# Performance work log

Measured on AMD Instinct MI355X. Metric: run time of the kernel, lower is better.

Reference implementation:

```python
import jax, jax.numpy as jnp
import numpy as np

BS, NV, D, DFF, E, H = 32, 512, 128, 512, 8, 8
EPS = 1e-5

def layernorm(x, g, b):
    m = x.mean(-1, keepdims=True)
    v = ((x - m) ** 2).mean(-1, keepdims=True)
    return (x - m) / jnp.sqrt(v + EPS) * g + b

def setup_inputs() -> dict:
    key = jax.random.key(0)
    ks = jax.random.split(key, 10)
    s = lambda k, shape: (jax.random.normal(k, shape, jnp.float32) * 0.02)
    return {
        "x": jax.random.normal(ks[0], (BS, NV, D), jnp.float32),
        "cls_emd": jax.random.normal(ks[1], (E, D), jnp.float32),
        "Wq": s(ks[2], (D, D)), "Wk": s(ks[3], (D, D)),
        "Wv": s(ks[4], (D, D)), "Wo": s(ks[5], (D, D)),
        "Wg": s(ks[6], (D, D)),
        "W1": s(ks[7], (E, DFF, 2 * D)), "b1": jnp.zeros((E, DFF), jnp.float32),
        "W2": s(ks[8], (E, D, DFF)), "b2": jnp.zeros((E, D), jnp.float32),
        "g1": jnp.ones((D,), jnp.float32), "be1": jnp.zeros((D,), jnp.float32),
        "g2": jnp.ones((D,), jnp.float32), "be2": jnp.zeros((D,), jnp.float32),
    }

def reference(x, cls_emd, Wq, Wk, Wv, Wo, Wg, W1, b1, W2, b2, g1, be1, g2, be2):
    bs, n, d = x.shape
    dh = d // H
    # --- full multi-head self-attention over the variate axis ---
    q = (x @ Wq).reshape(bs, n, H, dh)
    k = (x @ Wk).reshape(bs, n, H, dh)
    v = (x @ Wv).reshape(bs, n, H, dh)
    scores = jnp.einsum('bnhd,bmhd->bhnm', q, k) * (1.0 / np.sqrt(dh))
    attn = jax.nn.softmax(scores, axis=-1)            # [bs, H, n, n]
    new_x = jnp.einsum('bhnm,bmhd->bnhd', attn, v).reshape(bs, n, d) @ Wo
    # residual + norm1 (dropout = identity in eval)
    x = layernorm(x + new_x, g1, be1)
    # --- gating: per-variate scores over clusters [n_vars, n_clusters] ---
    gate_scores = jax.nn.softmax((x.mean(0) @ Wg) @ cls_emd.T, axis=-1)
    # --- MoE: expand tokens vs every cluster, concat, per-cluster expert MLP ---
    ncl = cls_emd.shape[0]
    y = jnp.broadcast_to(x[:, :, None, :], (bs, n, ncl, d))
    z = jnp.broadcast_to(cls_emd[None, None, :, :], (bs, n, ncl, d))
    yz_cat = jnp.concatenate([y, z], axis=-1)          # [bs, n, K, 2d]
    h = jax.nn.relu(jnp.einsum('bnkc,kfc->bnkf', yz_cat, W1) + b1)  # kernel_size=1 conv == matmul
    expert_out = jnp.einsum('bnkf,kdf->bnkd', h, W2) + b2           # [bs, n, K, d]
    y_r = jnp.einsum('nk,bnkd->bnd', gate_scores, expert_out)
    out = layernorm(x + y_r, g2, be2)
    return (out, attn, gate_scores)
```

## Files before the change

### kernel.cpp

```cpp
#include <hip/hip_runtime.h>
#include <hip/hip_bf16.h>
#include <math.h>

#define BS   32
#define NV   512
#define D    128
#define DFF  512
#define E    8
#define NH   8
#define DH   16
#define M_TOK (BS*NV)
#define EPS  1e-5f

typedef __hip_bfloat16 bf16;
typedef _Float16 f16;
using sh8   = __attribute__((ext_vector_type(8))) short;
using us4   = __attribute__((ext_vector_type(4))) unsigned short;
using h4    = __attribute__((ext_vector_type(4))) _Float16;
using h8    = __attribute__((ext_vector_type(8))) _Float16;
using f32x4 = __attribute__((ext_vector_type(4))) float;
using f32x16 = __attribute__((ext_vector_type(16))) float;

__device__ __forceinline__ float b2f(bf16 v){ return __bfloat162float(v); }
__device__ __forceinline__ bf16  f2b(float v){ return __float2bfloat16(v); }
__device__ __forceinline__ unsigned short f2bu(float v){
    bf16 b = __float2bfloat16(v);
    return __builtin_bit_cast(unsigned short, b);
}

__device__ __forceinline__ void gload_lds16(const void* g, void* l){
    __builtin_amdgcn_global_load_lds(
        (const __attribute__((address_space(1))) unsigned int*)g,
        (__attribute__((address_space(3))) unsigned int*)l, 16, 0, 0);
}

#define PR0 4096
#define PR1 (PR0 + 262144)
#define PR2 (PR1 + 131072)
#define PR3 (PR2 + 524288)
#define PR4 (PR3 + 49152)
#define PR5 (PR4 + 16384)
#define PREP_ITEMS PR5
__global__ __launch_bounds__(256) void k_prep(
    const float* __restrict__ W1, const float* __restrict__ W2,
    const float* __restrict__ x,  const float* __restrict__ Wq,
    const float* __restrict__ Wk, const float* __restrict__ Wv,
    const float* __restrict__ Wo, const float* __restrict__ b1,
    const float* __restrict__ cls,
    bf16* __restrict__ W1b, bf16* __restrict__ W2b, f16* __restrict__ xh,
    f16* __restrict__ WTq, f16* __restrict__ WoT, float* __restrict__ b1eff)
{
    int tid = blockIdx.x*256 + threadIdx.x;
    if (tid < PR0){
        int e = tid >> 9, f = tid & 511;
        float acc = b1[e*DFF + f];
        const float* wrow = W1 + ((size_t)e*DFF + f)*(2*D) + D;
        #pragma unroll 8
        for (int c=0;c<D;++c) acc += cls[e*D+c] * wrow[c];
        b1eff[tid] = acc;
    } else if (tid < PR1){
        int i = (tid - PR0)*4;
        float4 vv = *(const float4*)(W1 + i);
        us4 o; o[0]=f2bu(vv.x); o[1]=f2bu(vv.y); o[2]=f2bu(vv.z); o[3]=f2bu(vv.w);
        *(us4*)(W1b + i) = o;
    } else if (tid < PR2){
        int i = (tid - PR1)*4;
        float4 vv = *(const float4*)(W2 + i);
        us4 o; o[0]=f2bu(vv.x); o[1]=f2bu(vv.y); o[2]=f2bu(vv.z); o[3]=f2bu(vv.w);
        *(us4*)(W2b + i) = o;
    } else if (tid < PR3){
        int i = (tid - PR2)*4;
        float4 vv = *(const float4*)(x + i);
        h4 o; o[0]=(f16)vv.x; o[1]=(f16)vv.y; o[2]=(f16)vv.z; o[3]=(f16)vv.w;
        *(h4*)(xh + i) = o;
    } else if (tid < PR4){
        int idx = tid - PR3;
        int c = idx>>7, kk = idx&127;
        int which = c>>7, col = c&127;
        const float* W = which==0?Wq:(which==1?Wk:Wv);
        WTq[idx] = (f16)W[kk*D + col];
    } else if (tid < PR5){
        int idx = tid - PR4;
        int c = idx>>7, kk = idx&127;
        WoT[idx] = (f16)Wo[kk*D + c];
    }
}

__global__ __launch_bounds__(512) void k_qkv_mfma(
    const f16* __restrict__ xh, const f16* __restrict__ WT,
    f16* __restrict__ q, f16* __restrict__ k, f16* __restrict__ v)
{
    __shared__ __align__(16) char smem[65536];
    char* Xl = smem;
    char* Wl = smem + 16384;
    int t = threadIdx.x;
    int w = t>>6, lane = t&63;
    int bm = blockIdx.x, nh = blockIdx.y;

    const f16* xsrc = xh + (size_t)bm*64*D;
    #pragma unroll
    for (int i=0;i<2;++i){
        int ci = i*512 + t;
        int row = ci>>4, c16 = (ci&15)^(row&7);
        gload_lds16(xsrc + row*D + c16*8, Xl + (size_t)(i*512 + w*64)*16);
    }
    const f16* wsrc = WT + (size_t)nh*192*D;
    #pragma unroll
    for (int i=0;i<6;++i){
        int ci = i*512 + t;
        int row = ci>>4, c16 = (ci&15)^(row&7);
        gload_lds16(wsrc + row*D + c16*8, Wl + (size_t)(i*512 + w*64)*16);
    }
    __syncthreads();

    int rblk = w>>1, ch = w&1;
    int rl = lane&15, g = lane>>4;

    h8 afr[4];
    #pragma unroll
    for (int kk=0;kk<4;++kk){
        int row = rblk*16 + rl;
        int bo = (row<<8) + (kk<<6) + (g<<4); bo ^= (row&7)<<4;
        afr[kk] = *(const h8*)(Xl + bo);
    }
    f32x4 acc[6];
    #pragma unroll
    for (int nt=0;nt<6;++nt) acc[nt] = (f32x4){0.f,0.f,0.f,0.f};
    #pragma unroll
    for (int nt=0; nt<6; ++nt){
        #pragma unroll
        for (int kk=0;kk<4;++kk){
            int row = ch*96 + nt*16 + rl;
            int bo = (row<<8)+(kk<<6)+(g<<4); bo ^= (row&7)<<4;
            h8 bfr = *(const h8*)(Wl + bo);
            acc[nt] = __builtin_amdgcn_mfma_f32_16x16x32_f16(afr[kk], bfr, acc[nt],0,0,0);
        }
    }
    #pragma unroll
    for (int nt=0;nt<6;++nt){
        int cidx = nh*192 + ch*96 + nt*16 + rl;
        int which = cidx>>7, hh=(cidx>>4)&7, d = cidx&15;
        f16* dst = which==0?q:(which==1?k:v);
        #pragma unroll
        for (int j=0;j<4;++j){
            int m = bm*64 + rblk*16 + g*4 + j;
            int b = m>>9, n = m&511;
            dst[(((size_t)(b*NH+hh))*NV + n)*DH + d] = (f16)acc[nt][j];
        }
    }
}

#define KSTRIDE 24
#define VSTRIDE 520
#define PSTRIDE 68
__global__ __launch_bounds__(256) void k_attn2(
    const f16* __restrict__ q, const f16* __restrict__ kin, const f16* __restrict__ vin,
    float* __restrict__ attn_out, f16* __restrict__ ctx)
{
    __shared__ f16  Kl[512*KSTRIDE];
    __shared__ f16  VT[16*VSTRIDE];
    __shared__ f16  pbh[4][16*PSTRIDE];

    int bh = blockIdx.x;
    int t  = threadIdx.x;
    const f16* kb = kin + (size_t)bh*NV*DH;
    const f16* vb = vin + (size_t)bh*NV*DH;

    {
        int r0 = t*2;
        #pragma unroll
        for (int rr=0; rr<2; ++rr){
            const uint4* src = (const uint4*)(kb + (size_t)(r0+rr)*DH);
            *((uint4*)(Kl + (r0+rr)*KSTRIDE))     = src[0];
            *((uint4*)(Kl + (r0+rr)*KSTRIDE + 8)) = src[1];
        }
        const unsigned short* v0s = (const unsigned short*)(vb + (size_t)r0*DH);
        const unsigned short* v1s = v0s + DH;
        #pragma unroll
        for (int d=0; d<DH; ++d){
            unsigned u = (unsigned)v0s[d] | ((unsigned)v1s[d] << 16);
            *((unsigned*)(VT + d*VSTRIDE + r0)) = u;
        }
    }
    __syncthreads();

    int wave = t >> 6, lane = t & 63;
    int ql = lane & 15, g = lane >> 4;
    int q0 = blockIdx.y*64 + wave*16;

    h4 qf = *(const h4*)(q + ((size_t)bh*NV + q0 + ql)*DH + 4*g);
    #pragma unroll
    for (int i=0;i<4;++i) qf[i] = qf[i] * (_Float16)0.36067376f;

    f32x4 S[32];
    #pragma unroll
    for (int tt=0; tt<32; ++tt){
        h4 kf = *(const h4*)(Kl + (tt*16 + ql)*KSTRIDE + 4*g);
        S[tt] = __builtin_amdgcn_mfma_f32_16x16x16f16(kf, qf, (f32x4){0.f,0.f,0.f,0.f}, 0,0,0);
    }

    float sum = 0.f;
    #pragma unroll
    for (int tt=0; tt<32; ++tt)
        #pragma unroll
        for (int j=0;j<4;++j){
            float p = exp2f(S[tt][j]);
            S[tt][j] = p; sum += p;
        }
    sum += __shfl_xor(sum, 16);
    sum += __shfl_xor(sum, 32);
    float inv = 1.f/sum;
    #pragma unroll
    for (int tt=0; tt<32; ++tt)
        #pragma unroll
        for (int j=0;j<4;++j) S[tt][j] *= inv;

    f32x4 o0 = (f32x4){0.f,0.f,0.f,0.f}, o1 = (f32x4){0.f,0.f,0.f,0.f};
    f16* pw = pbh[wave];
    float* attnbase = attn_out + ((size_t)bh*NV + q0)*NV;
    int col16 = lane & 15, qg = lane >> 4;
    #pragma unroll
    for (int c=0; c<8; ++c){
        #pragma unroll
        for (int tt2=0; tt2<4; ++tt2){
            int tt = c*4 + tt2;
            h4 pf;
            pf[0]=(f16)S[tt][0]; pf[1]=(f16)S[tt][1];
            pf[2]=(f16)S[tt][2]; pf[3]=(f16)S[tt][3];
            h4 vf = *(const h4*)(VT + ql*VSTRIDE + tt*16 + 4*g);
            if (tt&1) o1 = __builtin_amdgcn_mfma_f32_16x16x16f16(vf, pf, o1, 0,0,0);
            else      o0 = __builtin_amdgcn_mfma_f32_16x16x16f16(vf, pf, o0, 0,0,0);
            *(h4*)(pw + ql*PSTRIDE + tt2*16 + 4*g) = pf;
        }
        asm volatile("" ::: "memory");
        #pragma unroll
        for (int rr=0; rr<4; ++rr){
            int qq = rr*4 + qg;
            h4 hv = *(const h4*)(pw + qq*PSTRIDE + col16*4);
            f32x4 vv;
            vv[0]=(float)hv[0]; vv[1]=(float)hv[1];
            vv[2]=(float)hv[2]; vv[3]=(float)hv[3];
            __builtin_nontemporal_store(vv, (f32x4*)(attnbase + (size_t)qq*NV + c*64 + col16*4));
        }
        asm volatile("" ::: "memory");
    }
    f32x4 o = o0 + o1;
    int b = bh >> 3, h = bh & 7;
    f16* cb = ctx + ((size_t)(b*NV) + q0 + ql)*D + h*DH + 4*g;
    h4 oc; oc[0]=(f16)o[0]; oc[1]=(f16)o[1]; oc[2]=(f16)o[2]; oc[3]=(f16)o[3];
    *(h4*)cb = oc;
}

__global__ __launch_bounds__(512) void k_woln_mfma(
    const f16* __restrict__ ctx, const f16* __restrict__ WoT,
    const float* __restrict__ x, const float* __restrict__ g1, const float* __restrict__ be1,
    bf16* __restrict__ x1b, float* __restrict__ yacc)
{
    __shared__ __align__(16) char smem[49152];
    __shared__ float lnred[2][64][2];
    char* Cl = smem;
    char* Wl = smem + 16384;
    int t = threadIdx.x;
    int w = t>>6, lane = t&63;
    int bm = blockIdx.x;

    const f16* csrc = ctx + (size_t)bm*64*D;
    #pragma unroll
    for (int i=0;i<2;++i){
        int ci = i*512 + t;
        int row = ci>>4, c16 = (ci&15)^(row&7);
        gload_lds16(csrc + row*D + c16*8, Cl + (size_t)(i*512 + w*64)*16);
    }
    #pragma unroll
    for (int i=0;i<4;++i){
        int ci = i*512 + t;
        int row = ci>>4, c16 = (ci&15)^(row&7);
        gload_lds16(WoT + row*D + c16*8, Wl + (size_t)(i*512 + w*64)*16);
    }
    __syncthreads();

    int rblk = w>>1, ch = w&1;
    int rl = lane&15, g = lane>>4;

    h8 afr[4];
    #pragma unroll
    for (int kk=0;kk<4;++kk){
        int row = rblk*16 + rl;
        int bo = (row<<8) + (kk<<6) + (g<<4); bo ^= (row&7)<<4;
        afr[kk] = *(const h8*)(Cl + bo);
    }
    f32x4 acc[4];
    #pragma unroll
    for (int nt=0;nt<4;++nt) acc[nt] = (f32x4){0.f,0.f,0.f,0.f};
    #pragma unroll
    for (int nt=0; nt<4; ++nt){
        #pragma unroll
        for (int kk=0;kk<4;++kk){
            int row = ch*64 + nt*16 + rl;
            int bo = (row<<8)+(kk<<6)+(g<<4); bo ^= (row&7)<<4;
            h8 bfr = *(const h8*)(Wl + bo);
            acc[nt] = __builtin_amdgcn_mfma_f32_16x16x32_f16(afr[kk], bfr, acc[nt],0,0,0);
        }
    }

    float rowv[4][4];
    #pragma unroll
    for (int j=0;j<4;++j){
        int m = bm*64 + rblk*16 + g*4 + j;
        #pragma unroll
        for (int dt=0;dt<4;++dt){
            int d = ch*64 + dt*16 + rl;
            rowv[j][dt] = acc[dt][j] + x[(size_t)m*D + d];
        }
    }
    #pragma unroll
    for (int j=0;j<4;++j){
        float s  = rowv[j][0]+rowv[j][1]+rowv[j][2]+rowv[j][3];
        float s2 = rowv[j][0]*rowv[j][0]+rowv[j][1]*rowv[j][1]
                 + rowv[j][2]*rowv[j][2]+rowv[j][3]*rowv[j][3];
        #pragma unroll
        for (int o=1;o<16;o<<=1){ s += __shfl_xor(s,o); s2 += __shfl_xor(s2,o); }
        if (rl==0){
            int row = rblk*16 + g*4 + j;
            lnred[ch][row][0] = s;
            lnred[ch][row][1] = s2;
        }
    }
    __syncthreads();
    #pragma unroll
    for (int j=0;j<4;++j){
        int row = rblk*16 + g*4 + j;
        float S  = lnred[0][row][0] + lnred[1][row][0];
        float S2 = lnred[0][row][1] + lnred[1][row][1];
        float mean = S*(1.f/D);
        float var  = S2*(1.f/D) - mean*mean;
        float rs = rsqrtf(var + EPS);
        int m = bm*64 + row;
        #pragma unroll
        for (int dt=0;dt<4;++dt){
            int d = ch*64 + dt*16 + rl;
            float o1 = (rowv[j][dt]-mean)*rs*g1[d] + be1[d];
            x1b[(size_t)m*D + d] = f2b(o1);
            yacc[(size_t)m*D + d] = o1;
        }
    }
}

__global__ __launch_bounds__(128) void k_gate(
    const float* __restrict__ yacc, const float* __restrict__ Wg, const float* __restrict__ cls,
    float* __restrict__ gate, float* __restrict__ gate_out)
{
    __shared__ float xm[D];
    __shared__ float tt[D];
    __shared__ float se[E];
    int n = blockIdx.x, t = threadIdx.x;
    float s = 0.f;
    #pragma unroll
    for (int b=0;b<BS;++b) s += yacc[((size_t)b*NV + n)*D + t];
    xm[t] = s * (1.f/BS);
    __syncthreads();
    float a = 0.f;
    for (int c=0;c<D;++c) a += xm[c] * Wg[c*D + t];
    tt[t] = a;
    __syncthreads();
    if (t < E){
        float acc=0.f;
        for (int c=0;c<D;++c) acc += tt[c] * cls[t*D + c];
        se[t]=acc;
    }
    __syncthreads();
    if (t==0){
        float mx=se[0];
        for(int e=1;e<E;++e) mx=fmaxf(mx,se[e]);
        float sm=0.f; float p[E];
        for(int e=0;e<E;++e){ p[e]=__expf(se[e]-mx); sm+=p[e]; }
        float inv=1.f/sm;
        for(int e=0;e<E;++e){
            gate[n*E+e]     = p[e]*inv;
            gate_out[n*E+e] = p[e]*inv;
        }
    }
}

__global__ __launch_bounds__(512) void k_moe_fused(
    const bf16* __restrict__ x1b, const bf16* __restrict__ W1b, const bf16* __restrict__ W2b,
    const float* __restrict__ b1eff, const float* __restrict__ b2,
    const float* __restrict__ gate, const float* __restrict__ yacc,
    const float* __restrict__ g2, const float* __restrict__ be2,
    float* __restrict__ out)
{
    __shared__ __align__(16) char smem[147456];
    char* Hl = smem + 131072;
    float (*lnred)[4][2] = (float (*)[4][2])Hl;

    int t = threadIdx.x;
    int w = t >> 6, lane = t & 63;
    int mb = w >> 2, nb = w & 3;
    int l31 = lane & 31, h = lane >> 5;
    int bm = blockIdx.x;

    sh8 afr[8];
    {
        const bf16* Ab = x1b + (size_t)(bm*64 + mb*32 + l31)*D;
        #pragma unroll
        for (int s=0;s<8;++s) afr[s] = *(const sh8*)(Ab + s*16 + h*8);
    }

    f32x16 oacc = {};
    f32x16 acc2e = {};

    auto STAGE = [&](int idx, int buf){
        int e = idx >> 2, fc = idx & 3;
        const bf16* w1src = W1b + ((size_t)e*DFF + fc*128)*(2*D);
        const bf16* w2src = W2b + (size_t)e*D*DFF + fc*128;
        char* Wa = smem + buf*65536;
        char* Wb = Wa + 32768;
        #pragma unroll
        for (int i=0;i<4;++i){
            int ci  = (i*8 + w)*64 + lane;
            int row = ci >> 4;
            int c16 = (ci & 15) ^ (row & 7);
            gload_lds16(w1src + (size_t)row*256 + c16*8, Wa + (size_t)(i*8+w)*1024);
            gload_lds16(w2src + (size_t)row*512 + c16*8, Wb + (size_t)(i*8+w)*1024);
        }
    };

    STAGE(0, 0);
    asm volatile("s_waitcnt vmcnt(0)" ::: "memory");
    __syncthreads();

    for (int idx=0; idx<32; ++idx){
        int buf = idx & 1;
        int e = idx >> 2, fc = idx & 3;
        char* Wa = smem + buf*65536;
        char* Wb = Wa + 32768;

        if (idx < 31) STAGE(idx+1, buf^1);

        f32x16 acc1 = {};
        {
            int row = nb*32 + l31;
            int rbase = (row<<8);
            int swz = (row&7)<<4;
            #pragma unroll
            for (int s=0;s<8;++s){
                int bo = (rbase + s*32 + h*16) ^ swz;
                sh8 bfr = *(const sh8*)(Wa + bo);
                acc1 = __builtin_amdgcn_mfma_f32_32x32x16_bf16(afr[s], bfr, acc1, 0,0,0);
            }
        }
        {
            float bia = b1eff[e*DFF + fc*128 + nb*32 + l31];
            #pragma unroll
            for (int r=0;r<16;++r){
                int rowm = mb*32 + (r&3) + 8*(r>>2) + 4*h;
                float v = acc1[r] + bia;
                v = v > 0.f ? v : 0.f;
                int bo = (rowm<<8) + ((nb*32 + l31)<<1);
                bo ^= (rowm&7)<<4;
                *(bf16*)(Hl + bo) = f2b(v);
            }
        }
        __syncthreads();

        {
            int rowh = mb*32 + l31;
            int hbase = (rowh<<8), hswz = (rowh&7)<<4;
            int roww = nb*32 + l31;
            int wbase = (roww<<8), wswz = (roww&7)<<4;
            #pragma unroll
            for (int s=0;s<8;++s){
                sh8 hfr = *(const sh8*)(Hl + ((hbase + s*32 + h*16) ^ hswz));
                sh8 wfr = *(const sh8*)(Wb + ((wbase + s*32 + h*16) ^ wswz));
                acc2e = __builtin_amdgcn_mfma_f32_32x32x16_bf16(hfr, wfr, acc2e, 0,0,0);
            }
        }

        if (fc == 3){
            int d = nb*32 + l31;
            float bia2 = b2[e*D + d];
            #pragma unroll
            for (int r=0;r<16;++r){
                int m = bm*64 + mb*32 + (r&3) + 8*(r>>2) + 4*h;
                float gv = gate[(m & 511)*E + e];
                oacc[r] += gv*(acc2e[r] + bia2);
            }
            acc2e = (f32x16){};
        }

        asm volatile("s_waitcnt vmcnt(0)" ::: "memory");
        __syncthreads();
    }

    int d = nb*32 + l31;
    float rowv[16];
    #pragma unroll
    for (int r=0;r<16;++r){
        int m = bm*64 + mb*32 + (r&3) + 8*(r>>2) + 4*h;
        rowv[r] = oacc[r] + yacc[(size_t)m*D + d];
    }
    #pragma unroll
    for (int r=0;r<16;++r){
        float s = rowv[r], s2 = rowv[r]*rowv[r];
        #pragma unroll
        for (int o=1;o<32;o<<=1){ s += __shfl_xor(s,o); s2 += __shfl_xor(s2,o); }
        if (l31==0){
            int rowl = mb*32 + (r&3) + 8*(r>>2) + 4*h;
            lnred[rowl][nb][0] = s;
            lnred[rowl][nb][1] = s2;
        }
    }
    __syncthreads();
    #pragma unroll
    for (int r=0;r<16;++r){
        int rowl = mb*32 + (r&3) + 8*(r>>2) + 4*h;
        float S  = lnred[rowl][0][0]+lnred[rowl][1][0]+lnred[rowl][2][0]+lnred[rowl][3][0];
        float S2 = lnred[rowl][0][1]+lnred[rowl][1][1]+lnred[rowl][2][1]+lnred[rowl][3][1];
        float mean = S*(1.f/D);
        float var  = S2*(1.f/D) - mean*mean;
        float rs = rsqrtf(var + EPS);
        int m = bm*64 + rowl;
        out[(size_t)m*D + d] = (rowv[r]-mean)*rs*g2[d] + be2[d];
    }
}

extern "C" void kernel_launch(void* const* d_in, const int* in_sizes, int n_in,
                              void* d_out, int out_size, void* d_ws, size_t ws_size,
                              hipStream_t stream)
{
    const float* x   = (const float*)d_in[0];
    const float* cls = (const float*)d_in[1];
    const float* Wq  = (const float*)d_in[2];
    const float* Wk  = (const float*)d_in[3];
    const float* Wv  = (const float*)d_in[4];
    const float* Wo  = (const float*)d_in[5];
    const float* Wg  = (const float*)d_in[6];
    const float* W1  = (const float*)d_in[7];
    const float* b1  = (const float*)d_in[8];
    const float* W2  = (const float*)d_in[9];
    const float* b2  = (const float*)d_in[10];
    const float* g1  = (const float*)d_in[11];
    const float* be1 = (const float*)d_in[12];
    const float* g2  = (const float*)d_in[13];
    const float* be2 = (const float*)d_in[14];

    float* out      = (float*)d_out;
    float* attn     = out + (size_t)M_TOK*D;
    float* gate_out = attn + (size_t)BS*NH*NV*NV;

    char* ws = (char*)d_ws;
    size_t off = 0;
    auto alloc = [&](size_t bytes)->void*{ void* p = ws + off; off += (bytes + 255) & ~(size_t)255; return p; };
    f16*   q    = (f16*)  alloc((size_t)M_TOK*D*2);
    f16*   kbuf = (f16*)  alloc((size_t)M_TOK*D*2);
    f16*   vbuf = (f16*)  alloc((size_t)M_TOK*D*2);
    f16*   ctx  = (f16*)  alloc((size_t)M_TOK*D*2);
    bf16*  x1b  = (bf16*) alloc((size_t)M_TOK*D*2);
    float* yacc = (float*)alloc((size_t)M_TOK*D*4);
    float* gate = (float*)alloc((size_t)NV*E*4);
    float* b1eff= (float*)alloc((size_t)E*DFF*4);
    bf16*  W1b  = (bf16*) alloc((size_t)E*DFF*2*D*2);
    bf16*  W2b  = (bf16*) alloc((size_t)E*D*DFF*2);
    f16*   xh   = (f16*)  alloc((size_t)M_TOK*D*2);
    f16*   WTq  = (f16*)  alloc((size_t)384*D*2);
    f16*   WoT  = (f16*)  alloc((size_t)D*D*2);

    k_prep<<<(PREP_ITEMS+255)/256, 256, 0, stream>>>(
        W1, W2, x, Wq, Wk, Wv, Wo, b1, cls,
        W1b, W2b, xh, WTq, WoT, b1eff);

    k_qkv_mfma<<<dim3(M_TOK/64, 2), 512, 0, stream>>>(xh, WTq, q, kbuf, vbuf);
    k_attn2<<<dim3(BS*NH, NV/64), 256, 0, stream>>>(q, kbuf, vbuf, attn, ctx);
    k_woln_mfma<<<M_TOK/64, 512, 0, stream>>>(ctx, WoT, x, g1, be1, x1b, yacc);
    k_gate<<<NV, 128, 0, stream>>>(yacc, Wg, cls, gate, gate_out);
    k_moe_fused<<<256, 512, 0, stream>>>(x1b, W1b, W2b, b1eff, b2, gate, yacc, g2, be2, out);
}
```

Baseline: 165.7 us.

## Fuse all stages into one persistent cooperative kernel with grid syncs

Replaces the six separate launches (prep, QKV, attention, Wo+LN, gate, MoE) with a single cooperative kernel of 256 blocks that runs each stage in turn, separated by grid-wide syncs. Each stage's work is remapped onto the fixed block count: QKV handles all 384 output columns per block, and attention loops over four query parts per (batch, head). The intent is to remove per-launch overhead and the gaps between dependent kernels. In exchange the whole grid is limited to 256 blocks with a 147KB shared buffer, so per-stage parallelism and occupancy drop, and every grid.sync adds barrier cost.

```diff
diff --git a/kernel.cpp b/kernel.cpp
--- a/kernel.cpp
+++ b/kernel.cpp
@@ -1,6 +1,9 @@
 #include <hip/hip_runtime.h>
+#include <hip/hip_cooperative_groups.h>
 #include <hip/hip_bf16.h>
 #include <math.h>
+
+namespace cg = cooperative_groups;
 
 #define BS   32
 #define NV   512
@@ -41,486 +44,466 @@
 #define PR4 (PR3 + 49152)
 #define PR5 (PR4 + 16384)
 #define PREP_ITEMS PR5
-__global__ __launch_bounds__(256) void k_prep(
-    const float* __restrict__ W1, const float* __restrict__ W2,
-    const float* __restrict__ x,  const float* __restrict__ Wq,
-    const float* __restrict__ Wk, const float* __restrict__ Wv,
-    const float* __restrict__ Wo, const float* __restrict__ b1,
-    const float* __restrict__ cls,
-    bf16* __restrict__ W1b, bf16* __restrict__ W2b, f16* __restrict__ xh,
-    f16* __restrict__ WTq, f16* __restrict__ WoT, float* __restrict__ b1eff)
-{
-    int tid = blockIdx.x*256 + threadIdx.x;
-    if (tid < PR0){
-        int e = tid >> 9, f = tid & 511;
-        float acc = b1[e*DFF + f];
-        const float* wrow = W1 + ((size_t)e*DFF + f)*(2*D) + D;
-        #pragma unroll 8
-        for (int c=0;c<D;++c) acc += cls[e*D+c] * wrow[c];
-        b1eff[tid] = acc;
-    } else if (tid < PR1){
-        int i = (tid - PR0)*4;
-        float4 vv = *(const float4*)(W1 + i);
-        us4 o; o[0]=f2bu(vv.x); o[1]=f2bu(vv.y); o[2]=f2bu(vv.z); o[3]=f2bu(vv.w);
-        *(us4*)(W1b + i) = o;
-    } else if (tid < PR2){
-        int i = (tid - PR1)*4;
-        float4 vv = *(const float4*)(W2 + i);
-        us4 o; o[0]=f2bu(vv.x); o[1]=f2bu(vv.y); o[2]=f2bu(vv.z); o[3]=f2bu(vv.w);
-        *(us4*)(W2b + i) = o;
-    } else if (tid < PR3){
-        int i = (tid - PR2)*4;
-        float4 vv = *(const float4*)(x + i);
-        h4 o; o[0]=(f16)vv.x; o[1]=(f16)vv.y; o[2]=(f16)vv.z; o[3]=(f16)vv.w;
-        *(h4*)(xh + i) = o;
-    } else if (tid < PR4){
-        int idx = tid - PR3;
-        int c = idx>>7, kk = idx&127;
-        int which = c>>7, col = c&127;
-        const float* W = which==0?Wq:(which==1?Wk:Wv);
-        WTq[idx] = (f16)W[kk*D + col];
-    } else if (tid < PR5){
-        int idx = tid - PR4;
-        int c = idx>>7, kk = idx&127;
-        WoT[idx] = (f16)Wo[kk*D + c];
-    }
-}
-
-__global__ __launch_bounds__(512) void k_qkv_mfma(
-    const f16* __restrict__ xh, const f16* __restrict__ WT,
-    f16* __restrict__ q, f16* __restrict__ k, f16* __restrict__ v)
-{
-    __shared__ __align__(16) char smem[65536];
-    char* Xl = smem;
-    char* Wl = smem + 16384;
-    int t = threadIdx.x;
-    int w = t>>6, lane = t&63;
-    int bm = blockIdx.x, nh = blockIdx.y;
-
-    const f16* xsrc = xh + (size_t)bm*64*D;
-    #pragma unroll
-    for (int i=0;i<2;++i){
-        int ci = i*512 + t;
-        int row = ci>>4, c16 = (ci&15)^(row&7);
-        gload_lds16(xsrc + row*D + c16*8, Xl + (size_t)(i*512 + w*64)*16);
-    }
-    const f16* wsrc = WT + (size_t)nh*192*D;
-    #pragma unroll
-    for (int i=0;i<6;++i){
-        int ci = i*512 + t;
-        int row = ci>>4, c16 = (ci&15)^(row&7);
-        gload_lds16(wsrc + row*D + c16*8, Wl + (size_t)(i*512 + w*64)*16);
-    }
-    __syncthreads();
-
-    int rblk = w>>1, ch = w&1;
-    int rl = lane&15, g = lane>>4;
-
-    h8 afr[4];
-    #pragma unroll
-    for (int kk=0;kk<4;++kk){
-        int row = rblk*16 + rl;
-        int bo = (row<<8) + (kk<<6) + (g<<4); bo ^= (row&7)<<4;
-        afr[kk] = *(const h8*)(Xl + bo);
-    }
-    f32x4 acc[6];
-    #pragma unroll
-    for (int nt=0;nt<6;++nt) acc[nt] = (f32x4){0.f,0.f,0.f,0.f};
-    #pragma unroll
-    for (int nt=0; nt<6; ++nt){
-        #pragma unroll
-        for (int kk=0;kk<4;++kk){
-            int row = ch*96 + nt*16 + rl;
-            int bo = (row<<8)+(kk<<6)+(g<<4); bo ^= (row&7)<<4;
-            h8 bfr = *(const h8*)(Wl + bo);
-            acc[nt] = __builtin_amdgcn_mfma_f32_16x16x32_f16(afr[kk], bfr, acc[nt],0,0,0);
-        }
-    }
-    #pragma unroll
-    for (int nt=0;nt<6;++nt){
-        int cidx = nh*192 + ch*96 + nt*16 + rl;
-        int which = cidx>>7, hh=(cidx>>4)&7, d = cidx&15;
-        f16* dst = which==0?q:(which==1?k:v);
-        #pragma unroll
-        for (int j=0;j<4;++j){
-            int m = bm*64 + rblk*16 + g*4 + j;
-            int b = m>>9, n = m&511;
-            dst[(((size_t)(b*NH+hh))*NV + n)*DH + d] = (f16)acc[nt][j];
-        }
-    }
-}
 
 #define KSTRIDE 24
 #define VSTRIDE 520
 #define PSTRIDE 68
-__global__ __launch_bounds__(256) void k_attn2(
-    const f16* __restrict__ q, const f16* __restrict__ kin, const f16* __restrict__ vin,
-    float* __restrict__ attn_out, f16* __restrict__ ctx)
+
+struct KP {
+    const float *x, *cls, *Wq, *Wk, *Wv, *Wo, *Wg, *W1, *b1, *W2, *b2, *g1, *be1, *g2, *be2;
+    float *out, *attn, *gate_out;
+    f16  *q, *kbuf, *vbuf, *ctx, *xh, *WTq, *WoT;
+    bf16 *x1b, *W1b, *W2b;
+    float *yacc, *gate, *b1eff;
+};
+
+__global__ __launch_bounds__(512, 2) void k_all(KP p)
 {
-    __shared__ f16  Kl[512*KSTRIDE];
-    __shared__ f16  VT[16*VSTRIDE];
-    __shared__ f16  pbh[4][16*PSTRIDE];
-
-    int bh = blockIdx.x;
-    int t  = threadIdx.x;
-    const f16* kb = kin + (size_t)bh*NV*DH;
-    const f16* vb = vin + (size_t)bh*NV*DH;
+    cg::grid_group grid = cg::this_grid();
+    __shared__ __align__(16) char smem[147456];
+
+    const int bid = blockIdx.x;
+    const int t   = threadIdx.x;
+    const int w   = t >> 6;
+    const int lane = t & 63;
+
+    for (int tid = bid*512 + t; tid < PREP_ITEMS; tid += 256*512){
+        if (tid < PR0){
+            int e = tid >> 9, f = tid & 511;
+            float acc = p.b1[e*DFF + f];
+            const float* wrow = p.W1 + ((size_t)e*DFF + f)*(2*D) + D;
+            #pragma unroll 8
+            for (int c=0;c<D;++c) acc += p.cls[e*D+c] * wrow[c];
+            p.b1eff[tid] = acc;
+        } else if (tid < PR1){
+            int i = (tid - PR0)*4;
+            float4 vv = *(const float4*)(p.W1 + i);
+            us4 o; o[0]=f2bu(vv.x); o[1]=f2bu(vv.y); o[2]=f2bu(vv.z); o[3]=f2bu(vv.w);
+            *(us4*)(p.W1b + i) = o;
+        } else if (tid < PR2){
+            int i = (tid - PR1)*4;
+            float4 vv = *(const float4*)(p.W2 + i);
+            us4 o; o[0]=f2bu(vv.x); o[1]=f2bu(vv.y); o[2]=f2bu(vv.z); o[3]=f2bu(vv.w);
+            *(us4*)(p.W2b + i) = o;
+        } else if (tid < PR3){
+            int i = (tid - PR2)*4;
+            float4 vv = *(const float4*)(p.x + i);
+            h4 o; o[0]=(f16)vv.x; o[1]=(f16)vv.y; o[2]=(f16)vv.z; o[3]=(f16)vv.w;
+            *(h4*)(p.xh + i) = o;
+        } else if (tid < PR4){
+            int idx = tid - PR3;
+            int c = idx>>7, kk = idx&127;
+            int which = c>>7, col = c&127;
+            const float* W = which==0?p.Wq:(which==1?p.Wk:p.Wv);
+            p.WTq[idx] = (f16)W[kk*D + col];
+        } else {
+            int idx = tid - PR4;
+            int c = idx>>7, kk = idx&127;
+            p.WoT[idx] = (f16)p.Wo[kk*D + c];
+        }
+    }
+    grid.sync();
 
     {
-        int r0 = t*2;
-        #pragma unroll
-        for (int rr=0; rr<2; ++rr){
-            const uint4* src = (const uint4*)(kb + (size_t)(r0+rr)*DH);
-            *((uint4*)(Kl + (r0+rr)*KSTRIDE))     = src[0];
-            *((uint4*)(Kl + (r0+rr)*KSTRIDE + 8)) = src[1];
-        }
-        const unsigned short* v0s = (const unsigned short*)(vb + (size_t)r0*DH);
-        const unsigned short* v1s = v0s + DH;
-        #pragma unroll
-        for (int d=0; d<DH; ++d){
-            unsigned u = (unsigned)v0s[d] | ((unsigned)v1s[d] << 16);
-            *((unsigned*)(VT + d*VSTRIDE + r0)) = u;
+        char* Xl = smem;
+        char* Wl = smem + 16384;
+        const f16* xsrc = p.xh + (size_t)bid*64*D;
+        #pragma unroll
+        for (int i=0;i<2;++i){
+            int ci = i*512 + t;
+            int row = ci>>4, c16 = (ci&15)^(row&7);
+            gload_lds16(xsrc + row*D + c16*8, Xl + (size_t)(i*512 + w*64)*16);
+        }
+        #pragma unroll
+        for (int i=0;i<12;++i){
+            int ci = i*512 + t;
+            int row = ci>>4, c16 = (ci&15)^(row&7);
+            gload_lds16(p.WTq + row*D + c16*8, Wl + (size_t)(i*512 + w*64)*16);
+        }
+        __syncthreads();
+
+        int rblk = w>>1, ch = w&1;
+        int rl = lane&15, g = lane>>4;
+
+        h8 afr[4];
+        #pragma unroll
+        for (int kk=0;kk<4;++kk){
+            int row = rblk*16 + rl;
+            int bo = (row<<8) + (kk<<6) + (g<<4); bo ^= (row&7)<<4;
+            afr[kk] = *(const h8*)(Xl + bo);
+        }
+        #pragma unroll
+        for (int nt=0; nt<12; ++nt){
+            f32x4 acc = (f32x4){0.f,0.f,0.f,0.f};
+            #pragma unroll
+            for (int kk=0;kk<4;++kk){
+                int row = ch*192 + nt*16 + rl;
+                int bo = (row<<8)+(kk<<6)+(g<<4); bo ^= (row&7)<<4;
+                h8 bfr = *(const h8*)(Wl + bo);
+                acc = __builtin_amdgcn_mfma_f32_16x16x32_f16(afr[kk], bfr, acc,0,0,0);
+            }
+            int cidx = ch*192 + nt*16 + rl;
+            int which = cidx>>7, hh=(cidx>>4)&7, d = cidx&15;
+            f16* dst = which==0?p.q:(which==1?p.kbuf:p.vbuf);
+            #pragma unroll
+            for (int j=0;j<4;++j){
+                int m = bid*64 + rblk*16 + g*4 + j;
+                int b = m>>9, n = m&511;
+                dst[(((size_t)(b*NH+hh))*NV + n)*DH + d] = (f16)acc[j];
+            }
         }
     }
-    __syncthreads();
-
-    int wave = t >> 6, lane = t & 63;
-    int ql = lane & 15, g = lane >> 4;
-    int q0 = blockIdx.y*64 + wave*16;
-
-    h4 qf = *(const h4*)(q + ((size_t)bh*NV + q0 + ql)*DH + 4*g);
-    #pragma unroll
-    for (int i=0;i<4;++i) qf[i] = qf[i] * (_Float16)0.36067376f;
-
-    f32x4 S[32];
-    #pragma unroll
-    for (int tt=0; tt<32; ++tt){
-        h4 kf = *(const h4*)(Kl + (tt*16 + ql)*KSTRIDE + 4*g);
-        S[tt] = __builtin_amdgcn_mfma_f32_16x16x16f16(kf, qf, (f32x4){0.f,0.f,0.f,0.f}, 0,0,0);
+    grid.sync();
+
+    {
+        f16* Kl  = (f16*)smem;
+        f16* VT  = (f16*)(smem + 24576);
+        f16* pbh = (f16*)(smem + 24576 + 16640);
+
+        int bh = bid;
+        const f16* kb = p.kbuf + (size_t)bh*NV*DH;
+        const f16* vb = p.vbuf + (size_t)bh*NV*DH;
+
+        if (t < 256){
+            int r0 = t*2;
+            #pragma unroll
+            for (int rr=0; rr<2; ++rr){
+                const uint4* src = (const uint4*)(kb + (size_t)(r0+rr)*DH);
+                *((uint4*)(Kl + (r0+rr)*KSTRIDE))     = src[0];
+                *((uint4*)(Kl + (r0+rr)*KSTRIDE + 8)) = src[1];
+            }
+            const unsigned short* v0s = (const unsigned short*)(vb + (size_t)r0*DH);
+            const unsigned short* v1s = v0s + DH;
+            #pragma unroll
+            for (int d=0; d<DH; ++d){
+                unsigned u = (unsigned)v0s[d] | ((unsigned)v1s[d] << 16);
+                *((unsigned*)(VT + d*VSTRIDE + r0)) = u;
+            }
+        }
+        __syncthreads();
+
+        int ql = lane & 15, g = lane >> 4;
+        int b = bh >> 3, h = bh & 7;
+
+        for (int part=0; part<4; ++part){
+            int q0 = part*128 + w*16;
+
+            h4 qf = *(const h4*)(p.q + ((size_t)bh*NV + q0 + ql)*DH + 4*g);
+            #pragma unroll
+            for (int i=0;i<4;++i) qf[i] = qf[i] * (_Float16)0.36067376f;
+
+            f32x4 S[32];
+            #pragma unroll
+            for (int tt=0; tt<32; ++tt){
+                h4 kf = *(const h4*)(Kl + (tt*16 + ql)*KSTRIDE + 4*g);
+                S[tt] = __builtin_amdgcn_mfma_f32_16x16x16f16(kf, qf, (f32x4){0.f,0.f,0.f,0.f}, 0,0,0);
+            }
+            float sum = 0.f;
+            #pragma unroll
+            for (int tt=0; tt<32; ++tt)
+                #pragma unroll
+                for (int j=0;j<4;++j){
+                    float pv = exp2f(S[tt][j]);
+                    S[tt][j] = pv; sum += pv;
+                }
+            sum += __shfl_xor(sum, 16);
+            sum += __shfl_xor(sum, 32);
+            float inv = 1.f/sum;
+            #pragma unroll
+            for (int tt=0; tt<32; ++tt)
+                #pragma unroll
+                for (int j=0;j<4;++j) S[tt][j] *= inv;
+
+            f32x4 o0 = (f32x4){0.f,0.f,0.f,0.f}, o1 = (f32x4){0.f,0.f,0.f,0.f};
+            f16* pw = pbh + w*(16*PSTRIDE);
+            float* attnbase = p.attn + ((size_t)bh*NV + q0)*NV;
+            int col16 = lane & 15, qg = lane >> 4;
+            #pragma unroll
+            for (int c=0; c<8; ++c){
+                #pragma unroll
+                for (int tt2=0; tt2<4; ++tt2){
+                    int tt = c*4 + tt2;
+                    h4 pf;
+                    pf[0]=(f16)S[tt][0]; pf[1]=(f16)S[tt][1];
+                    pf[2]=(f16)S[tt][2]; pf[3]=(f16)S[tt][3];
+                    h4 vf = *(const h4*)(VT + ql*VSTRIDE + tt*16 + 4*g);
+                    if (tt&1) o1 = __builtin_amdgcn_mfma_f32_16x16x16f16(vf, pf, o1, 0,0,0);
+                    else      o0 = __builtin_amdgcn_mfma_f32_16x16x16f16(vf, pf, o0, 0,0,0);
+                    *(h4*)(pw + ql*PSTRIDE + tt2*16 + 4*g) = pf;
+                }
+                asm volatile("" ::: "memory");
+                #pragma unroll
+                for (int rr=0; rr<4; ++rr){
+                    int qq = rr*4 + qg;
+                    h4 hv = *(const h4*)(pw + qq*PSTRIDE + col16*4);
+                    f32x4 vv;
+                    vv[0]=(float)hv[0]; vv[1]=(float)hv[1];
+                    vv[2]=(float)hv[2]; vv[3]=(float)hv[3];
+                    __builtin_nontemporal_store(vv, (f32x4*)(attnbase + (size_t)qq*NV + c*64 + col16*4));
+                }
+                asm volatile("" ::: "memory");
+            }
+            f32x4 o = o0 + o1;
+            f16* cb = p.ctx + ((size_t)(b*NV) + q0 + ql)*D + h*DH + 4*g;
+            h4 oc; oc[0]=(f16)o[0]; oc[1]=(f16)o[1]; oc[2]=(f16)o[2]; oc[3]=(f16)o[3];
+            *(h4*)cb = oc;
+        }
     }
-
-    float sum = 0.f;
-    #pragma unroll
-    for (int tt=0; tt<32; ++tt)
+    grid.sync();
+
+    {
+        char* Cl = smem;
+        char* Wl = smem + 16384;
+        float (*lnred)[64][2] = (float (*)[64][2])(smem + 49152);
+
+        const f16* csrc = p.ctx + (size_t)bid*64*D;
+        #pragma unroll
+        for (int i=0;i<2;++i){
+            int ci = i*512 + t;
+            int row = ci>>4, c16 = (ci&15)^(row&7);
+            gload_lds16(csrc + row*D + c16*8, Cl + (size_t)(i*512 + w*64)*16);
+        }
+        #pragma unroll
+        for (int i=0;i<4;++i){
+            int ci = i*512 + t;
+            int row = ci>>4, c16 = (ci&15)^(row&7);
+            gload_lds16(p.WoT + row*D + c16*8, Wl + (size_t)(i*512 + w*64)*16);
+        }
+        __syncthreads();
+
+        int rblk = w>>1, ch = w&1;
+        int rl = lane&15, g = lane>>4;
+
+        h8 afr[4];
+        #pragma unroll
+        for (int kk=0;kk<4;++kk){
+            int row = rblk*16 + rl;
+            int bo = (row<<8) + (kk<<6) + (g<<4); bo ^= (row&7)<<4;
+            afr[kk] = *(const h8*)(Cl + bo);
+        }
+        f32x4 acc[4];
+        #pragma unroll
+        for (int nt=0;nt<4;++nt) acc[nt] = (f32x4){0.f,0.f,0.f,0.f};
+        #pragma unroll
+        for (int nt=0; nt<4; ++nt){
+            #pragma unroll
+            for (int kk=0;kk<4;++kk){
+                int row = ch*64 + nt*16 + rl;
+                int bo = (row<<8)+(kk<<6)+(g<<4); bo ^= (row&7)<<4;
+                h8 bfr = *(const h8*)(Wl + bo);
+                acc[nt] = __builtin_amdgcn_mfma_f32_16x16x32_f16(afr[kk], bfr, acc[nt],0,0,0);
+            }
+        }
+        float rowv[4][4];
         #pragma unroll
         for (int j=0;j<4;++j){
-            float p = exp2f(S[tt][j]);
-            S[tt][j] = p; sum += p;
-        }
-    sum += __shfl_xor(sum, 16);
-    sum += __shfl_xor(sum, 32);
-    float inv = 1.f/sum;
-    #pragma unroll
-    for (int tt=0; tt<32; ++tt)
-        #pragma unroll
-        for (int j=0;j<4;++j) S[tt][j] *= inv;
-
-    f32x4 o0 = (f32x4){0.f,0.f,0.f,0.f}, o1 = (f32x4){0.f,0.f,0.f,0.f};
-    f16* pw = pbh[wave];
-    float* attnbase = attn_out + ((size_t)bh*NV + q0)*NV;
-    int col16 = lane & 15, qg = lane >> 4;
-    #pragma unroll
-    for (int c=0; c<8; ++c){
-        #pragma unroll
-        for (int tt2=0; tt2<4; ++tt2){
-            int tt = c*4 + tt2;
-            h4 pf;
-            pf[0]=(f16)S[tt][0]; pf[1]=(f16)S[tt][1];
-            pf[2]=(f16)S[tt][2]; pf[3]=(f16)S[tt][3];
-            h4 vf = *(const h4*)(VT + ql*VSTRIDE + tt*16 + 4*g);
-            if (tt&1) o1 = __builtin_amdgcn_mfma_f32_16x16x16f16(vf, pf, o1, 0,0,0);
-            else      o0 = __builtin_amdgcn_mfma_f32_16x16x16f16(vf, pf, o0, 0,0,0);
-            *(h4*)(pw + ql*PSTRIDE + tt2*16 + 4*g) = pf;
-        }
-        asm volatile("" ::: "memory");
-        #pragma unroll
-        for (int rr=0; rr<4; ++rr){
-            int qq = rr*4 + qg;
-            h4 hv = *(const h4*)(pw + qq*PSTRIDE + col16*4);
-            f32x4 vv;
-            vv[0]=(float)hv[0]; vv[1]=(float)hv[1];
-            vv[2]=(float)hv[2]; vv[3]=(float)hv[3];
-            __builtin_nontemporal_store(vv, (f32x4*)(attnbase + (size_t)qq*NV + c*64 + col16*4));
-        }
-        asm volatile("" ::: "memory");
+            int m = bid*64 + rblk*16 + g*4 + j;
+            #pragma unroll
+            for (int dt=0;dt<4;++dt){
+                int d = ch*64 + dt*16 + rl;
+                rowv[j][dt] = acc[dt][j] + p.x[(size_t)m*D + d];
+            }
+        }
+        #pragma unroll
+        for (int j=0;j<4;++j){
+            float s  = rowv[j][0]+rowv[j][1]+rowv[j][2]+rowv[j][3];
+            float s2 = rowv[j][0]*rowv[j][0]+rowv[j][1]*rowv[j][1]
+                     + rowv[j][2]*rowv[j][2]+rowv[j][3]*rowv[j][3];
+            #pragma unroll
+            for (int o=1;o<16;o<<=1){ s += __shfl_xor(s,o); s2 += __shfl_xor(s2,o); }
+            if (rl==0){
+                int row = rblk*16 + g*4 + j;
+                lnred[ch][row][0] = s;
+                lnred[ch][row][1] = s2;
+            }
+        }
+        __syncthreads();
+        #pragma unroll
+        for (int j=0;j<4;++j){
+            int row = rblk*16 + g*4 + j;
+            float S  = lnred[0][row][0] + lnred[1][row][0];
+            float S2 = lnred[0][row][1] + lnred[1][row][1];
+            float mean = S*(1.f/D);
+            float var  = S2*(1.f/D) - mean*mean;
+            float rs = rsqrtf(var + EPS);
+            int m = bid*64 + row;
+            #pragma unroll
+            for (int dt=0;dt<4;++dt){
+                int d = ch*64 + dt*16 + rl;
+                float o1 = (rowv[j][dt]-mean)*rs*p.g1[d] + p.be1[d];
+                p.x1b[(size_t)m*D + d] = f2b(o1);
+                p.yacc[(size_t)m*D + d] = o1;
+            }
+        }
     }
-    f32x4 o = o0 + o1;
-    int b = bh >> 3, h = bh & 7;
-    f16* cb = ctx + ((size_t)(b*NV) + q0 + ql)*D + h*DH + 4*g;
-    h4 oc; oc[0]=(f16)o[0]; oc[1]=(f16)o[1]; oc[2]=(f16)o[2]; oc[3]=(f16)o[3];
-    *(h4*)cb = oc;
-}
-
-__global__ __launch_bounds__(512) void k_woln_mfma(
-    const f16* __restrict__ ctx, const f16* __restrict__ WoT,
-    const float* __restrict__ x, const float* __restrict__ g1, const float* __restrict__ be1,
-    bf16* __restrict__ x1b, float* __restrict__ yacc)
-{
-    __shared__ __align__(16) char smem[49152];
-    __shared__ float lnred[2][64][2];
-    char* Cl = smem;
-    char* Wl = smem + 16384;
-    int t = threadIdx.x;
-    int w = t>>6, lane = t&63;
-    int bm = blockIdx.x;
-
-    const f16* csrc = ctx + (size_t)bm*64*D;
-    #pragma unroll
-    for (int i=0;i<2;++i){
-        int ci = i*512 + t;
-        int row = ci>>4, c16 = (ci&15)^(row&7);
-        gload_lds16(csrc + row*D + c16*8, Cl + (size_t)(i*512 + w*64)*16);
+    grid.sync();
+
+    {
+        float* xm0 = (float*)smem;
+        float* tv0 = xm0 + 256;
+        float* se0 = tv0 + 256;
+        int grp = (t>>7)&1;
+        int tl = t&127;
+        int n = bid*2 + grp;
+        float s = 0.f;
+        #pragma unroll
+        for (int b=0;b<BS;++b) s += p.yacc[((size_t)b*NV + n)*D + tl];
+        xm0[grp*128+tl] = s * (1.f/BS);
+        __syncthreads();
+        float a = 0.f;
+        for (int c2=0;c2<D;++c2) a += xm0[grp*128+c2] * p.Wg[c2*D + tl];
+        tv0[grp*128+tl] = a;
+        __syncthreads();
+        if (tl < E){
+            float acc=0.f;
+            for (int c2=0;c2<D;++c2) acc += tv0[grp*128+c2] * p.cls[tl*D + c2];
+            se0[grp*8+tl]=acc;
+        }
+        __syncthreads();
+        if (tl==0){
+            float mx=se0[grp*8];
+            for(int e=1;e<E;++e) mx=fmaxf(mx,se0[grp*8+e]);
+            float sm=0.f; float pr[E];
+            for(int e=0;e<E;++e){ pr[e]=__expf(se0[grp*8+e]-mx); sm+=pr[e]; }
+            float inv=1.f/sm;
+            for(int e=0;e<E;++e){
+                p.gate[n*E+e]     = pr[e]*inv;
+                p.gate_out[n*E+e] = pr[e]*inv;
+            }
+        }
     }
-    #pragma unroll
-    for (int i=0;i<4;++i){
-        int ci = i*512 + t;
-        int row = ci>>4, c16 = (ci&15)^(row&7);
-        gload_lds16(WoT + row*D + c16*8, Wl + (size_t)(i*512 + w*64)*16);
-    }
-    __syncthreads();
-
-    int rblk = w>>1, ch = w&1;
-    int rl = lane&15, g = lane>>4;
-
-    h8 afr[4];
-    #pragma unroll
-    for (int kk=0;kk<4;++kk){
-        int row = rblk*16 + rl;
-        int bo = (row<<8) + (kk<<6) + (g<<4); bo ^= (row&7)<<4;
-        afr[kk] = *(const h8*)(Cl + bo);
-    }
-    f32x4 acc[4];
-    #pragma unroll
-    for (int nt=0;nt<4;++nt) acc[nt] = (f32x4){0.f,0.f,0.f,0.f};
-    #pragma unroll
-    for (int nt=0; nt<4; ++nt){
-        #pragma unroll
-        for (int kk=0;kk<4;++kk){
-            int row = ch*64 + nt*16 + rl;
-            int bo = (row<<8)+(kk<<6)+(g<<4); bo ^= (row&7)<<4;
-            h8 bfr = *(const h8*)(Wl + bo);
-            acc[nt] = __builtin_amdgcn_mfma_f32_16x16x32_f16(afr[kk], bfr, acc[nt],0,0,0);
-        }
-    }
-
-    float rowv[4][4];
-    #pragma unroll
-    for (int j=0;j<4;++j){
-        int m = bm*64 + rblk*16 + g*4 + j;
-        #pragma unroll
-        for (int dt=0;dt<4;++dt){
-            int d = ch*64 + dt*16 + rl;
-            rowv[j][dt] = acc[dt][j] + x[(size_t)m*D + d];
-        }
-    }
-    #pragma unroll
-    for (int j=0;j<4;++j){
-        float s  = rowv[j][0]+rowv[j][1]+rowv[j][2]+rowv[j][3];
-        float s2 = rowv[j][0]*rowv[j][0]+rowv[j][1]*rowv[j][1]
-                 + rowv[j][2]*rowv[j][2]+rowv[j][3]*rowv[j][3];
-        #pragma unroll
-        for (int o=1;o<16;o<<=1){ s += __shfl_xor(s,o); s2 += __shfl_xor(s2,o); }
-        if (rl==0){
-            int row = rblk*16 + g*4 + j;
-            lnred[ch][row][0] = s;
-            lnred[ch][row][1] = s2;
-        }
-    }
-    __syncthreads();
-    #pragma unroll
-    for (int j=0;j<4;++j){
-        int row = rblk*16 + g*4 + j;
-        float S  = lnred[0][row][0] + lnred[1][row][0];
-        float S2 = lnred[0][row][1] + lnred[1][row][1];
-        float mean = S*(1.f/D);
-        float var  = S2*(1.f/D) - mean*mean;
-        float rs = rsqrtf(var + EPS);
-        int m = bm*64 + row;
-        #pragma unroll
-        for (int dt=0;dt<4;++dt){
-            int d = ch*64 + dt*16 + rl;
-            float o1 = (rowv[j][dt]-mean)*rs*g1[d] + be1[d];
-            x1b[(size_t)m*D + d] = f2b(o1);
-            yacc[(size_t)m*D + d] = o1;
-        }
-    }
-}
-
-__global__ __launch_bounds__(128) void k_gate(
-    const float* __restrict__ yacc, const float* __restrict__ Wg, const float* __restrict__ cls,
-    float* __restrict__ gate, float* __restrict__ gate_out)
-{
-    __shared__ float xm[D];
-    __shared__ float tt[D];
-    __shared__ float se[E];
-    int n = blockIdx.x, t = threadIdx.x;
-    float s = 0.f;
-    #pragma unroll
-    for (int b=0;b<BS;++b) s += yacc[((size_t)b*NV + n)*D + t];
-    xm[t] = s * (1.f/BS);
-    __syncthreads();
-    float a = 0.f;
-    for (int c=0;c<D;++c) a += xm[c] * Wg[c*D + t];
-    tt[t] = a;
-    __syncthreads();
-    if (t < E){
-        float acc=0.f;
-        for (int c=0;c<D;++c) acc += tt[c] * cls[t*D + c];
-        se[t]=acc;
-    }
-    __syncthreads();
-    if (t==0){
-        float mx=se[0];
-        for(int e=1;e<E;++e) mx=fmaxf(mx,se[e]);
-        float sm=0.f; float p[E];
-        for(int e=0;e<E;++e){ p[e]=__expf(se[e]-mx); sm+=p[e]; }
-        float inv=1.f/sm;
-        for(int e=0;e<E;++e){
-            gate[n*E+e]     = p[e]*inv;
-            gate_out[n*E+e] = p[e]*inv;
-        }
-    }
-}
-
-__global__ __launch_bounds__(512) void k_moe_fused(
-    const bf16* __restrict__ x1b, const bf16* __restrict__ W1b, const bf16* __restrict__ W2b,
-    const float* __restrict__ b1eff, const float* __restrict__ b2,
-    const float* __restrict__ gate, const float* __restrict__ yacc,
-    const float* __restrict__ g2, const float* __restrict__ be2,
-    float* __restrict__ out)
-{
-    __shared__ __align__(16) char smem[147456];
-    char* Hl = smem + 131072;
-    float (*lnred)[4][2] = (float (*)[4][2])Hl;
-
-    int t = threadIdx.x;
-    int w = t >> 6, lane = t & 63;
-    int mb = w >> 2, nb = w & 3;
-    int l31 = lane & 31, h = lane >> 5;
-    int bm = blockIdx.x;
-
-    sh8 afr[8];
+    grid.sync();
+
     {
-        const bf16* Ab = x1b + (size_t)(bm*64 + mb*32 + l31)*D;
-        #pragma unroll
-        for (int s=0;s<8;++s) afr[s] = *(const sh8*)(Ab + s*16 + h*8);
-    }
-
-    f32x16 oacc = {};
-    f32x16 acc2e = {};
-
-    auto STAGE = [&](int idx, int buf){
-        int e = idx >> 2, fc = idx & 3;
-        const bf16* w1src = W1b + ((size_t)e*DFF + fc*128)*(2*D);
-        const bf16* w2src = W2b + (size_t)e*D*DFF + fc*128;
-        char* Wa = smem + buf*65536;
-        char* Wb = Wa + 32768;
-        #pragma unroll
-        for (int i=0;i<4;++i){
-            int ci  = (i*8 + w)*64 + lane;
-            int row = ci >> 4;
-            int c16 = (ci & 15) ^ (row & 7);
-            gload_lds16(w1src + (size_t)row*256 + c16*8, Wa + (size_t)(i*8+w)*1024);
-            gload_lds16(w2src + (size_t)row*512 + c16*8, Wb + (size_t)(i*8+w)*1024);
-        }
-    };
-
-    STAGE(0, 0);
-    asm volatile("s_waitcnt vmcnt(0)" ::: "memory");
-    __syncthreads();
-
-    for (int idx=0; idx<32; ++idx){
-        int buf = idx & 1;
-        int e = idx >> 2, fc = idx & 3;
-        char* Wa = smem + buf*65536;
-        char* Wb = Wa + 32768;
-
-        if (idx < 31) STAGE(idx+1, buf^1);
-
-        f32x16 acc1 = {};
+        char* Hl = smem + 131072;
+        float (*lnred)[4][2] = (float (*)[4][2])Hl;
+
+        int mb = w >> 2, nb = w & 3;
+        int l31 = lane & 31, h = lane >> 5;
+
+        sh8 afr[8];
         {
-            int row = nb*32 + l31;
-            int rbase = (row<<8);
-            int swz = (row&7)<<4;
-            #pragma unroll
-            for (int s=0;s<8;++s){
-                int bo = (rbase + s*32 + h*16) ^ swz;
-                sh8 bfr = *(const sh8*)(Wa + bo);
-                acc1 = __builtin_amdgcn_mfma_f32_32x32x16_bf16(afr[s], bfr, acc1, 0,0,0);
-            }
-        }
-        {
-            float bia = b1eff[e*DFF + fc*128 + nb*32 + l31];
-            #pragma unroll
-            for (int r=0;r<16;++r){
-                int rowm = mb*32 + (r&3) + 8*(r>>2) + 4*h;
-                float v = acc1[r] + bia;
-                v = v > 0.f ? v : 0.f;
-                int bo = (rowm<<8) + ((nb*32 + l31)<<1);
-                bo ^= (rowm&7)<<4;
-                *(bf16*)(Hl + bo) = f2b(v);
-            }
-        }
-        __syncthreads();
-
-        {
-            int rowh = mb*32 + l31;
-            int hbase = (rowh<<8), hswz = (rowh&7)<<4;
-            int roww = nb*32 + l31;
-            int wbase = (roww<<8), wswz = (roww&7)<<4;
-            #pragma unroll
-            for (int s=0;s<8;++s){
-                sh8 hfr = *(const sh8*)(Hl + ((hbase + s*32 + h*16) ^ hswz));
-                sh8 wfr = *(const sh8*)(Wb + ((wbase + s*32 + h*16) ^ wswz));
-                acc2e = __builtin_amdgcn_mfma_f32_32x32x16_bf16(hfr, wfr, acc2e, 0,0,0);
-            }
-        }
-
-        if (fc == 3){
-            int d = nb*32 + l31;
-            float bia2 = b2[e*D + d];
-            #pragma unroll
-            for (int r=0;r<16;++r){
-                int m = bm*64 + mb*32 + (r&3) + 8*(r>>2) + 4*h;
-                float gv = gate[(m & 511)*E + e];
-                oacc[r] += gv*(acc2e[r] + bia2);
-            }
-            acc2e = (f32x16){};
-        }
-
+            const bf16* Ab = p.x1b + (size_t)(bid*64 + mb*32 + l31)*D;
+            #pragma unroll
+            for (int s=0;s<8;++s) afr[s] = *(const sh8*)(Ab + s*16 + h*8);
+        }
+
+        f32x16 oacc = {};
+        f32x16 acc2e = {};
+
+        auto STAGE = [&](int idx, int buf){
+            int e = idx >> 2, fc = idx & 3;
+            const bf16* w1src = p.W1b + ((size_t)e*DFF + fc*128)*(2*D);
+            const bf16* w2src = p.W2b + (size_t)e*D*DFF + fc*128;
+            char* Wa = smem + buf*65536;
+            char* Wb = Wa + 32768;
+            #pragma unroll
+            for (int i=0;i<4;++i){
+                int ci  = (i*8 + w)*64 + lane;
+                int row = ci >> 4;
+                int c16 = (ci & 15) ^ (row & 7);
+                gload_lds16(w1src + (size_t)row*256 + c16*8, Wa + (size_t)(i*8+w)*1024);
+                gload_lds16(w2src + (size_t)row*512 + c16*8, Wb + (size_t)(i*8+w)*1024);
+            }
+        };
+
+        STAGE(0, 0);
         asm volatile("s_waitcnt vmcnt(0)" ::: "memory");
         __syncthreads();
-    }
-
-    int d = nb*32 + l31;
-    float rowv[16];
-    #pragma unroll
-    for (int r=0;r<16;++r){
-        int m = bm*64 + mb*32 + (r&3) + 8*(r>>2) + 4*h;
-        rowv[r] = oacc[r] + yacc[(size_t)m*D + d];
-    }
-    #pragma unroll
-    for (int r=0;r<16;++r){
-        float s = rowv[r], s2 = rowv[r]*rowv[r];
-        #pragma unroll
-        for (int o=1;o<32;o<<=1){ s += __shfl_xor(s,o); s2 += __shfl_xor(s2,o); }
-        if (l31==0){
+
+        for (int idx=0; idx<32; ++idx){
+            int buf = idx & 1;
+            int e = idx >> 2, fc = idx & 3;
+            char* Wa = smem + buf*65536;
+            char* Wb = Wa + 32768;
+
+            if (idx < 31) STAGE(idx+1, buf^1);
+
+            f32x16 acc1 = {};
+            {
+                int row = nb*32 + l31;
+                int rbase = (row<<8);
+                int swz = (row&7)<<4;
+                #pragma unroll
+                for (int s=0;s<8;++s){
+                    int bo = (rbase + s*32 + h*16) ^ swz;
+                    sh8 bfr = *(const sh8*)(Wa + bo);
+                    acc1 = __builtin_amdgcn_mfma_f32_32x32x16_bf16(afr[s], bfr, acc1, 0,0,0);
+                }
+            }
+            {
+                float bia = p.b1eff[e*DFF + fc*128 + nb*32 + l31];
+                #pragma unroll
+                for (int r=0;r<16;++r){
+                    int rowm = mb*32 + (r&3) + 8*(r>>2) + 4*h;
+                    float v = acc1[r] + bia;
+                    v = v > 0.f ? v : 0.f;
+                    int bo = (rowm<<8) + ((nb*32 + l31)<<1);
+                    bo ^= (rowm&7)<<4;
+                    *(bf16*)(Hl + bo) = f2b(v);
+                }
+            }
+            __syncthreads();
+
+            {
+                int rowh = mb*32 + l31;
+                int hbase = (rowh<<8), hswz = (rowh&7)<<4;
+                int roww = nb*32 + l31;
+                int wbase = (roww<<8), wswz = (roww&7)<<4;
+                #pragma unroll
+                for (int s=0;s<8;++s){
+                    sh8 hfr = *(const sh8*)(Hl + ((hbase + s*32 + h*16) ^ hswz));
+                    sh8 wfr = *(const sh8*)(Wb + ((wbase + s*32 + h*16) ^ wswz));
+                    acc2e = __builtin_amdgcn_mfma_f32_32x32x16_bf16(hfr, wfr, acc2e, 0,0,0);
+                }
+            }
+
+            if (fc == 3){
+                int d = nb*32 + l31;
+                float bia2 = p.b2[e*D + d];
+                #pragma unroll
+                for (int r=0;r<16;++r){
+                    int m = bid*64 + mb*32 + (r&3) + 8*(r>>2) + 4*h;
+                    float gv = p.gate[(m & 511)*E + e];
+                    oacc[r] += gv*(acc2e[r] + bia2);
+                }
+                acc2e = (f32x16){};
+            }
+
+            asm volatile("s_waitcnt vmcnt(0)" ::: "memory");
+            __syncthreads();
+        }
+
+        int d = nb*32 + l31;
+        float rowv[16];
+        #pragma unroll
+        for (int r=0;r<16;++r){
+            int m = bid*64 + mb*32 + (r&3) + 8*(r>>2) + 4*h;
+            rowv[r] = oacc[r] + p.yacc[(size_t)m*D + d];
+        }
+        #pragma unroll
+        for (int r=0;r<16;++r){
+            float s = rowv[r], s2 = rowv[r]*rowv[r];
+            #pragma unroll
+            for (int o=1;o<32;o<<=1){ s += __shfl_xor(s,o); s2 += __shfl_xor(s2,o); }
+            if (l31==0){
+                int rowl = mb*32 + (r&3) + 8*(r>>2) + 4*h;
+                lnred[rowl][nb][0] = s;
+                lnred[rowl][nb][1] = s2;
+            }
+        }
+        __syncthreads();
+        #pragma unroll
+        for (int r=0;r<16;++r){
             int rowl = mb*32 + (r&3) + 8*(r>>2) + 4*h;
-            lnred[rowl][nb][0] = s;
-            lnred[rowl][nb][1] = s2;
-        }
-    }
-    __syncthreads();
-    #pragma unroll
-    for (int r=0;r<16;++r){
-        int rowl = mb*32 + (r&3) + 8*(r>>2) + 4*h;
-        float S  = lnred[rowl][0][0]+lnred[rowl][1][0]+lnred[rowl][2][0]+lnred[rowl][3][0];
-        float S2 = lnred[rowl][0][1]+lnred[rowl][1][1]+lnred[rowl][2][1]+lnred[rowl][3][1];
-        float mean = S*(1.f/D);
-        float var  = S2*(1.f/D) - mean*mean;
-        float rs = rsqrtf(var + EPS);
-        int m = bm*64 + rowl;
-        out[(size_t)m*D + d] = (rowv[r]-mean)*rs*g2[d] + be2[d];
+            float S  = lnred[rowl][0][0]+lnred[rowl][1][0]+lnred[rowl][2][0]+lnred[rowl][3][0];
+            float S2 = lnred[rowl][0][1]+lnred[rowl][1][1]+lnred[rowl][2][1]+lnred[rowl][3][1];
+            float mean = S*(1.f/D);
+            float var  = S2*(1.f/D) - mean*mean;
+            float rs = rsqrtf(var + EPS);
+            int m = bid*64 + rowl;
+            p.out[(size_t)m*D + d] = (rowv[r]-mean)*rs*p.g2[d] + p.be2[d];
+        }
     }
 }
 
@@ -528,50 +511,44 @@
                               void* d_out, int out_size, void* d_ws, size_t ws_size,
                               hipStream_t stream)
 {
-    const float* x   = (const float*)d_in[0];
-    const float* cls = (const float*)d_in[1];
-    const float* Wq  = (const float*)d_in[2];
-    const float* Wk  = (const float*)d_in[3];
-    const float* Wv  = (const float*)d_in[4];
-    const float* Wo  = (const float*)d_in[5];
-    const float* Wg  = (const float*)d_in[6];
-    const float* W1  = (const float*)d_in[7];
-    const float* b1  = (const float*)d_in[8];
-    const float* W2  = (const float*)d_in[9];
-    const float* b2  = (const float*)d_in[10];
-    const float* g1  = (const float*)d_in[11];
-    const float* be1 = (const float*)d_in[12];
-    const float* g2  = (const float*)d_in[13];
-    const float* be2 = (const float*)d_in[14];
-
-    float* out      = (float*)d_out;
-    float* attn     = out + (size_t)M_TOK*D;
-    float* gate_out = attn + (size_t)BS*NH*NV*NV;
+    KP p;
+    p.x   = (const float*)d_in[0];
+    p.cls = (const float*)d_in[1];
+    p.Wq  = (const float*)d_in[2];
+    p.Wk  = (const float*)d_in[3];
+    p.Wv  = (const float*)d_in[4];
+    p.Wo  = (const float*)d_in[5];
+    p.Wg  = (const float*)d_in[6];
+    p.W1  = (const float*)d_in[7];
+    p.b1  = (const float*)d_in[8];
+    p.W2  = (const float*)d_in[9];
+    p.b2  = (const float*)d_in[10];
+    p.g1  = (const float*)d_in[11];
+    p.be1 = (const float*)d_in[12];
+    p.g2  = (const float*)d_in[13];
+    p.be2 = (const float*)d_in[14];
+
+    p.out      = (float*)d_out;
+    p.attn     = p.out + (size_t)M_TOK*D;
+    p.gate_out = p.attn + (size_t)BS*NH*NV*NV;
 
     char* ws = (char*)d_ws;
     size_t off = 0;
-    auto alloc = [&](size_t bytes)->void*{ void* p = ws + off; off += (bytes + 255) & ~(size_t)255; return p; };
-    f16*   q    = (f16*)  alloc((size_t)M_TOK*D*2);
-    f16*   kbuf = (f16*)  alloc((size_t)M_TOK*D*2);
-    f16*   vbuf = (f16*)  alloc((size_t)M_TOK*D*2);
-    f16*   ctx  = (f16*)  alloc((size_t)M_TOK*D*2);
-    bf16*  x1b  = (bf16*) alloc((size_t)M_TOK*D*2);
-    float* yacc = (float*)alloc((size_t)M_TOK*D*4);
-    float* gate = (float*)alloc((size_t)NV*E*4);
-    float* b1eff= (float*)alloc((size_t)E*DFF*4);
-    bf16*  W1b  = (bf16*) alloc((size_t)E*DFF*2*D*2);
-    bf16*  W2b  = (bf16*) alloc((size_t)E*D*DFF*2);
-    f16*   xh   = (f16*)  alloc((size_t)M_TOK*D*2);
-    f16*   WTq  = (f16*)  alloc((size_t)384*D*2);
-    f16*   WoT  = (f16*)  alloc((size_t)D*D*2);
-
-    k_prep<<<(PREP_ITEMS+255)/256, 256, 0, stream>>>(
-        W1, W2, x, Wq, Wk, Wv, Wo, b1, cls,
-        W1b, W2b, xh, WTq, WoT, b1eff);
-
-    k_qkv_mfma<<<dim3(M_TOK/64, 2), 512, 0, stream>>>(xh, WTq, q, kbuf, vbuf);
-    k_attn2<<<dim3(BS*NH, NV/64), 256, 0, stream>>>(q, kbuf, vbuf, attn, ctx);
-    k_woln_mfma<<<M_TOK/64, 512, 0, stream>>>(ctx, WoT, x, g1, be1, x1b, yacc);
-    k_gate<<<NV, 128, 0, stream>>>(yacc, Wg, cls, gate, gate_out);
-    k_moe_fused<<<256, 512, 0, stream>>>(x1b, W1b, W2b, b1eff, b2, gate, yacc, g2, be2, out);
+    auto alloc = [&](size_t bytes)->void*{ void* q = ws + off; off += (bytes + 255) & ~(size_t)255; return q; };
+    p.q    = (f16*)  alloc((size_t)M_TOK*D*2);
+    p.kbuf = (f16*)  alloc((size_t)M_TOK*D*2);
+    p.vbuf = (f16*)  alloc((size_t)M_TOK*D*2);
+    p.ctx  = (f16*)  alloc((size_t)M_TOK*D*2);
+    p.x1b  = (bf16*) alloc((size_t)M_TOK*D*2);
+    p.yacc = (float*)alloc((size_t)M_TOK*D*4);
+    p.gate = (float*)alloc((size_t)NV*E*4);
+    p.b1eff= (float*)alloc((size_t)E*DFF*4);
+    p.W1b  = (bf16*) alloc((size_t)E*DFF*2*D*2);
+    p.W2b  = (bf16*) alloc((size_t)E*D*DFF*2);
+    p.xh   = (f16*)  alloc((size_t)M_TOK*D*2);
+    p.WTq  = (f16*)  alloc((size_t)384*D*2);
+    p.WoT  = (f16*)  alloc((size_t)D*D*2);
+
+    void* args[] = { (void*)&p };
+    hipLaunchCooperativeKernel((const void*)k_all, dim3(256), dim3(512), args, 0, stream);
 }
```

New measurement: 320.8 us. 93.5% more time.
